# Kernel tuning notes

Hardware: AMD Instinct MI355X
Metric: run time of the kernel (lower is better)

## Reference

```python
import jax, jax.numpy as jnp
import numpy as np

NUM_CLS = 80
SR = 0.2
STRIDES = (8, 16, 32, 64, 128)
IMG = 1280
FMAPS = [(IMG // s, IMG // s) for s in STRIDES]
MAX_BOXES = 128
BIG_AREA = 1e7  # padding value for box-area argmin (matches tf.pad constant)


def _shrink_boxes(boxes, fw, fh, stride, sr):
    # shrink gt boxes by `sr` around their center and snap to feature-grid ints
    b = boxes / stride
    cx = (b[:, 0] + b[:, 2]) * 0.5
    cy = (b[:, 1] + b[:, 3]) * 0.5
    hw = (b[:, 2] - b[:, 0]) * sr * 0.5
    hh = (b[:, 3] - b[:, 1]) * sr * 0.5
    px1 = jnp.clip(jnp.floor(cx - hw), 0, fw - 1).astype(jnp.int32)
    py1 = jnp.clip(jnp.floor(cy - hh), 0, fh - 1).astype(jnp.int32)
    px2 = jnp.clip(jnp.ceil(cx + hw).astype(jnp.int32), px1 + 1, fw)
    py2 = jnp.clip(jnp.ceil(cy + hh).astype(jnp.int32), py1 + 1, fh)
    return px1, py1, px2, py2


def _level_targets(boxes, labels, valid, sel_w, fh, fw, stride):
    # Vectorized replacement of the per-box tf.map_fn + tf.pad + argmin + gather_nd.
    # The original builds a padded dense map per box; padding values are:
    #   cls one-hot -> 0, soft weight -> 1, regr mask -> 0, regr target -> 0, area -> 1e7.
    # We instead compute dense [K,fh,fw] maps and mask, which is the same math.
    px1, py1, px2, py2 = _shrink_boxes(boxes, fw, fh, stride, SR)  # [K]
    sx = (jnp.arange(fw, dtype=jnp.float32) + 0.5) * stride  # pixel-center x
    sy = (jnp.arange(fh, dtype=jnp.float32) + 0.5) * stride  # pixel-center y
    dl = jnp.maximum(sx[None, None, :] - boxes[:, 0, None, None], 0.0)  # [K,fh,fw]
    dt = jnp.maximum(sy[None, :, None] - boxes[:, 1, None, None], 0.0)
    dr = jnp.maximum(boxes[:, 2, None, None] - sx[None, None, :], 0.0)
    db = jnp.maximum(boxes[:, 3, None, None] - sy[None, :, None], 0.0)
    gx = jnp.arange(fw)[None, None, :]
    gy = jnp.arange(fh)[None, :, None]
    in_box = ((gx >= px1[:, None, None]) & (gx < px2[:, None, None])
              & (gy >= py1[:, None, None]) & (gy < py2[:, None, None])
              & valid[:, None, None])  # [K,fh,fw] positive region per box
    area = jnp.where(in_box, (dl + dr) * (dt + db), BIG_AREA)
    win = jnp.argmin(area, axis=0)  # [fh,fw] smallest-area box per pixel

    take = lambda a: jnp.take_along_axis(a, win[None], axis=0)[0]
    is_pos = take(in_box).astype(jnp.float32)
    dl_w, dt_w, dr_w, db_w = take(dl), take(dt), take(dr), take(db)

    # anchor-point weight min/max ratio (guard 0/0 which is only hit off-target)
    num = jnp.minimum(dl_w, dr_w) * jnp.minimum(dt_w, db_w)
    den = jnp.maximum(dl_w, dr_w) * jnp.maximum(dt_w, db_w)
    ap = jnp.where(den > 0, num / jnp.maximum(den, 1e-12), 0.0)
    soft = jnp.where(is_pos > 0, ap * sel_w[win], 1.0)

    onehot = jax.nn.one_hot(labels[win], NUM_CLS, dtype=jnp.float32) * is_pos[..., None]
    regr = (jnp.stack([dl_w, dt_w, dr_w, db_w], axis=-1) / (4.0 * stride)) * is_pos[..., None]
    extra = jnp.stack([soft, is_pos], axis=-1)  # [fh,fw,2] soft weight + pos mask
    cls_t = jnp.concatenate([onehot, extra], axis=-1).reshape(fh * fw, NUM_CLS + 2)
    regr_t = jnp.concatenate([regr, extra], axis=-1).reshape(fh * fw, 4 + 2)
    return cls_t, regr_t


def reference(gt_boxes, feature_select_weight, feature_maps_shape):
    # feature_maps_shape is accepted for signature fidelity; shapes must be
    # static under jit so we use the FMAPS constant (same values).
    labels = gt_boxes[:, 4].astype(jnp.int32)
    boxes = gt_boxes[:, :4]
    valid = jnp.any(jnp.abs(boxes) > 0, axis=1)  # trim_zero_padding_boxes as mask
    cls_list, regr_list = [], []
    for lvl, stride in enumerate(STRIDES):
        fh, fw = FMAPS[lvl]
        c, r = _level_targets(boxes, labels, valid,
                              feature_select_weight[:, lvl], fh, fw, stride)
        cls_list.append(c)
        regr_list.append(r)
    return jnp.concatenate(cls_list, axis=0), jnp.concatenate(regr_list, axis=0)


def setup_inputs():
    key = jax.random.key(0)
    k1, k2, k3, k4 = jax.random.split(key, 4)
    xy = jax.random.uniform(k1, (MAX_BOXES, 2), minval=0.0, maxval=IMG - 64.0)
    wh = jax.random.uniform(k2, (MAX_BOXES, 2), minval=32.0, maxval=420.0)
    x2y2 = jnp.minimum(xy + wh, IMG - 1.0)
    labels = jax.random.randint(k3, (MAX_BOXES, 1), 0, NUM_CLS).astype(jnp.float32)
    gt = jnp.concatenate([xy, x2y2, labels], axis=-1)
    # zero out last quarter to exercise the zero-padding trim path
    pad_mask = (jnp.arange(MAX_BOXES) < MAX_BOXES * 3 // 4).astype(jnp.float32)
    gt = gt * pad_mask[:, None]
    fsw = jax.random.uniform(k4, (MAX_BOXES, len(STRIDES)))
    fshape = jnp.array(FMAPS, dtype=jnp.int32)
    return {"gt_boxes": gt, "feature_select_weight": fsw,
            "feature_maps_shape": fshape}
```

## Files before the change

kernel.cpp:

```cpp
#include <hip/hip_runtime.h>
#include <math.h>
#include <limits.h>

#define NUM_CLS   80
#define MAX_BOXES 128
#define NLVL      5
#define BIG_AREA  1.0e7f
#define TOTAL_PIX 34100
#define PPB       128

__global__ __launch_bounds__(256) void fcos_targets_kernel(
    const float* __restrict__ gt,
    const float* __restrict__ fsw,
    float* __restrict__ out_cls,
    float* __restrict__ out_reg)
{
    __shared__ float4 sbx[MAX_BOXES];
    __shared__ int4   sshr[MAX_BOXES][NLVL];
    __shared__ float  ssw[MAX_BOXES][NLVL];
    __shared__ int    slab[MAX_BOXES];
    __shared__ float  pbest[PPB];
    __shared__ int    pwin[PPB];
    __shared__ float  st_soft[PPB];
    __shared__ float  st_ispos[PPB];
    __shared__ int    st_lab[PPB];
    __shared__ float  st_reg[PPB][4];

    const int t = threadIdx.x;
    const int block_base = blockIdx.x * PPB;
    const int block_last = min(block_base + PPB, TOTAL_PIX) - 1;

    const int lvl_lo = (block_base < 25600) ? 0 : (block_base < 32000) ? 1 :
                       (block_base < 33600) ? 2 : (block_base < 34000) ? 3 : 4;
    const int lvl_hi = (block_last < 25600) ? 0 : (block_last < 32000) ? 1 :
                       (block_last < 33600) ? 2 : (block_last < 34000) ? 3 : 4;

    if (t < MAX_BOXES) {
        const float x1 = gt[t * 5 + 0];
        const float y1 = gt[t * 5 + 1];
        const float x2 = gt[t * 5 + 2];
        const float y2 = gt[t * 5 + 3];
        sbx[t]  = make_float4(x1, y1, x2, y2);
        slab[t] = (int)gt[t * 5 + 4];
        const bool valid = (fabsf(x1) > 0.f) || (fabsf(y1) > 0.f) ||
                           (fabsf(x2) > 0.f) || (fabsf(y2) > 0.f);
        for (int l = lvl_lo; l <= lvl_hi; ++l) {
            const float inv_s = 1.0f / (float)(8 << l);
            const int   fw    = 160 >> l;
            const float fwm1  = (float)(fw - 1);
            const float bx1 = x1 * inv_s, by1 = y1 * inv_s;
            const float bx2 = x2 * inv_s, by2 = y2 * inv_s;
            const float cx = (bx1 + bx2) * 0.5f;
            const float cy = (by1 + by2) * 0.5f;
            const float hw = ((bx2 - bx1) * 0.2f) * 0.5f;
            const float hh = ((by2 - by1) * 0.2f) * 0.5f;
            int px1 = (int)fminf(fmaxf(floorf(cx - hw), 0.f), fwm1);
            int py1 = (int)fminf(fmaxf(floorf(cy - hh), 0.f), fwm1);
            int px2 = min(max((int)ceilf(cx + hw), px1 + 1), fw);
            int py2 = min(max((int)ceilf(cy + hh), py1 + 1), fw);
            if (!valid) { px1 = INT_MAX; py1 = INT_MAX; px2 = 0; py2 = 0; }
            sshr[t][l] = make_int4(px1, py1, px2, py2);
        }
    } else {
        const int b = t - MAX_BOXES;
        #pragma unroll
        for (int l = 0; l < NLVL; ++l) ssw[b][l] = fsw[b * NLVL + l];
    }
    __syncthreads();

    const int count = min(PPB, TOTAL_PIX - block_base);
    const int p   = t & (PPB - 1);
    const int pid = block_base + p;
    const bool active = (p < count);

    float best = BIG_AREA;
    int   win  = (t < PPB) ? 0 : 64;
    int   lvl = 0, gx = 0, gy = 0;
    float sx = 0.f, sy = 0.f;

    if (active) {
        int fw, lp; float stride;
        if      (pid < 25600) { lvl = 0; fw = 160; lp = pid;         stride = 8.f;   }
        else if (pid < 32000) { lvl = 1; fw = 80;  lp = pid - 25600; stride = 16.f;  }
        else if (pid < 33600) { lvl = 2; fw = 40;  lp = pid - 32000; stride = 32.f;  }
        else if (pid < 34000) { lvl = 3; fw = 20;  lp = pid - 33600; stride = 64.f;  }
        else                  { lvl = 4; fw = 10;  lp = pid - 34000; stride = 128.f; }
        gy = lp / fw;
        gx = lp - gy * fw;
        sx = ((float)gx + 0.5f) * stride;
        sy = ((float)gy + 0.5f) * stride;

        const int i0 = (t < PPB) ? 0 : 64;
        for (int j = 0; j < 64; ++j) {
            const int i = i0 + j;
            const int4  s = sshr[i][lvl];
            const float4 b = sbx[i];
            const bool inb = (gx >= s.x) & (gx < s.z) & (gy >= s.y) & (gy < s.w);
            const float dl = fmaxf(sx - b.x, 0.f);
            const float dt = fmaxf(sy - b.y, 0.f);
            const float dr = fmaxf(b.z - sx, 0.f);
            const float db = fmaxf(b.w - sy, 0.f);
            const float area = inb ? (dl + dr) * (dt + db) : BIG_AREA;
            if (area < best) { best = area; win = i; }
        }
    }
    if (t >= PPB) { pbest[p] = best; pwin[p] = win; }
    __syncthreads();

    if (t < PPB && active) {
        const float b2 = pbest[p];
        if (b2 < best) { best = b2; win = pwin[p]; }

        const int4   s = sshr[win][lvl];
        const float4 b = sbx[win];
        const bool inb = (gx >= s.x) & (gx < s.z) & (gy >= s.y) & (gy < s.w);
        const float dl = fmaxf(sx - b.x, 0.f);
        const float dt = fmaxf(sy - b.y, 0.f);
        const float dr = fmaxf(b.z - sx, 0.f);
        const float db = fmaxf(b.w - sy, 0.f);

        const float is_pos = inb ? 1.0f : 0.0f;
        const float num = fminf(dl, dr) * fminf(dt, db);
        const float den = fmaxf(dl, dr) * fmaxf(dt, db);
        const float ap  = (den > 0.f) ? num / fmaxf(den, 1e-12f) : 0.0f;
        const float soft = inb ? ap * ssw[win][lvl] : 1.0f;

        const float rs = 0.25f / (float)(8 << lvl);
        st_soft[p]  = soft;
        st_ispos[p] = is_pos;
        st_lab[p]   = slab[win];
        st_reg[p][0] = dl * rs * is_pos;
        st_reg[p][1] = dt * rs * is_pos;
        st_reg[p][2] = dr * rs * is_pos;
        st_reg[p][3] = db * rs * is_pos;
    }
    __syncthreads();

    if (count == PPB) {
        float4* cp = (float4*)(out_cls + (size_t)block_base * (NUM_CLS + 2));
        for (int q = t; q < PPB * (NUM_CLS + 2) / 4; q += 256) {
            const int flat = q * 4;
            const int row0 = (int)((unsigned)flat / 82u);
            const int col0 = flat - row0 * 82;
            float v[4];
            #pragma unroll
            for (int k = 0; k < 4; ++k) {
                int r = row0, c = col0 + k;
                if (c >= 82) { c -= 82; ++r; }
                const float ip = st_ispos[r];
                float val;
                if (c < NUM_CLS)       val = (c == st_lab[r] && ip != 0.f) ? 1.0f : 0.0f;
                else if (c == NUM_CLS) val = st_soft[r];
                else                   val = ip;
                v[k] = val;
            }
            cp[q] = make_float4(v[0], v[1], v[2], v[3]);
        }
        float4* rp = (float4*)(out_reg + (size_t)block_base * 6);
        for (int q = t; q < PPB * 6 / 4; q += 256) {
            const int flat = q * 4;
            const int row0 = (int)((unsigned)flat / 6u);
            const int col0 = flat - row0 * 6;
            float v[4];
            #pragma unroll
            for (int k = 0; k < 4; ++k) {
                int r = row0, c = col0 + k;
                if (c >= 6) { c -= 6; ++r; }
                v[k] = (c < 4) ? st_reg[r][c] : ((c == 4) ? st_soft[r] : st_ispos[r]);
            }
            rp[q] = make_float4(v[0], v[1], v[2], v[3]);
        }
    } else {
        float* cbase = out_cls + (size_t)block_base * (NUM_CLS + 2);
        for (int q = t; q < count * (NUM_CLS + 2); q += 256) {
            const int r = (int)((unsigned)q / 82u);
            const int c = q - r * 82;
            const float ip = st_ispos[r];
            float val;
            if (c < NUM_CLS)       val = (c == st_lab[r] && ip != 0.f) ? 1.0f : 0.0f;
            else if (c == NUM_CLS) val = st_soft[r];
            else                   val = ip;
            cbase[q] = val;
        }
        float* rbase = out_reg + (size_t)block_base * 6;
        for (int q = t; q < count * 6; q += 256) {
            const int r = (int)((unsigned)q / 6u);
            const int c = q - r * 6;
            rbase[q] = (c < 4) ? st_reg[r][c] : ((c == 4) ? st_soft[r] : st_ispos[r]);
        }
    }
}

extern "C" void kernel_launch(void* const* d_in, const int* in_sizes, int n_in,
                              void* d_out, int out_size, void* d_ws, size_t ws_size,
                              hipStream_t stream) {
    (void)in_sizes; (void)n_in; (void)out_size; (void)d_ws; (void)ws_size;
    const float* gt  = (const float*)d_in[0];
    const float* fsw = (const float*)d_in[1];
    float* out_cls = (float*)d_out;
    float* out_reg = out_cls + (size_t)TOTAL_PIX * (NUM_CLS + 2);

    const int blocks = (TOTAL_PIX + PPB - 1) / PPB;
    fcos_targets_kernel<<<blocks, 256, 0, stream>>>(gt, fsw, out_cls, out_reg);
}
```

Before: 70.83 us.

## Replace per-pixel box scan with box-to-pixel atomicMin scatter

Instead of each pixel testing all 128 boxes, each (box, level) pair scatters its shrunk region's areas into a workspace via 64-bit atomicMin on a packed (area, box index) key. A gather kernel then reads the winning box per pixel and writes outputs. This removes the dense K×pixels scan, since shrunk regions are small, but adds two extra kernel launches, a workspace init pass and atomic traffic. Ties resolve to the lowest box index, which matches argmin.

```diff
diff --git a/kernel.cpp b/kernel.cpp
--- a/kernel.cpp
+++ b/kernel.cpp
@@ -9,18 +9,90 @@
 #define TOTAL_PIX 34100
 #define PPB       128
 
-__global__ __launch_bounds__(256) void fcos_targets_kernel(
+#define INIT_KEY  0x4B18968000000000ULL
+
+__device__ __forceinline__ int level_base(int lvl) {
+    switch (lvl) {
+        case 0:  return 0;
+        case 1:  return 25600;
+        case 2:  return 32000;
+        case 3:  return 33600;
+        default: return 34000;
+    }
+}
+
+__global__ __launch_bounds__(256) void init_winner(unsigned long long* __restrict__ w) {
+    const int i = blockIdx.x * 256 + threadIdx.x;
+    if (i < TOTAL_PIX) w[i] = INIT_KEY;
+}
+
+__global__ __launch_bounds__(256) void scatter_kernel(
+    const float* __restrict__ gt,
+    unsigned long long* __restrict__ w)
+{
+    const int gtid = blockIdx.x * 256 + threadIdx.x;
+    const int pair = gtid >> 6;
+    const int lane = threadIdx.x & 63;
+    if (pair >= MAX_BOXES * NLVL) return;
+    const int box = pair & (MAX_BOXES - 1);
+    const int lvl = pair >> 7;
+
+    const float x1 = gt[box * 5 + 0];
+    const float y1 = gt[box * 5 + 1];
+    const float x2 = gt[box * 5 + 2];
+    const float y2 = gt[box * 5 + 3];
+    const bool valid = (fabsf(x1) > 0.f) || (fabsf(y1) > 0.f) ||
+                       (fabsf(x2) > 0.f) || (fabsf(y2) > 0.f);
+    if (!valid) return;
+
+    const float stride = (float)(8 << lvl);
+    const float inv_s  = 1.0f / stride;
+    const int   fw     = 160 >> lvl;
+    const float fwm1   = (float)(fw - 1);
+
+    const float bx1 = x1 * inv_s, by1 = y1 * inv_s;
+    const float bx2 = x2 * inv_s, by2 = y2 * inv_s;
+    const float cx = (bx1 + bx2) * 0.5f;
+    const float cy = (by1 + by2) * 0.5f;
+    const float hw = ((bx2 - bx1) * 0.2f) * 0.5f;
+    const float hh = ((by2 - by1) * 0.2f) * 0.5f;
+    const int px1 = (int)fminf(fmaxf(floorf(cx - hw), 0.f), fwm1);
+    const int py1 = (int)fminf(fmaxf(floorf(cy - hh), 0.f), fwm1);
+    const int px2 = min(max((int)ceilf(cx + hw), px1 + 1), fw);
+    const int py2 = min(max((int)ceilf(cy + hh), py1 + 1), fw);
+
+    const int rw = px2 - px1;
+    const int n  = rw * (py2 - py1);
+    const int base = level_base(lvl);
+
+    for (int i = lane; i < n; i += 64) {
+        const int ry = i / rw;
+        const int rx = i - ry * rw;
+        const int gx = px1 + rx;
+        const int gy = py1 + ry;
+        const float sx = ((float)gx + 0.5f) * stride;
+        const float sy = ((float)gy + 0.5f) * stride;
+        const float dl = fmaxf(sx - x1, 0.f);
+        const float dt = fmaxf(sy - y1, 0.f);
+        const float dr = fmaxf(x2 - sx, 0.f);
+        const float db = fmaxf(y2 - sy, 0.f);
+        const float area = (dl + dr) * (dt + db);
+        const unsigned long long key =
+            ((unsigned long long)__float_as_uint(area) << 32) | (unsigned)box;
+        atomicMin(&w[base + gy * fw + gx], key);
+    }
+}
+
+__global__ __launch_bounds__(256) void gather_kernel(
     const float* __restrict__ gt,
     const float* __restrict__ fsw,
+    const unsigned long long* __restrict__ w,
     float* __restrict__ out_cls,
     float* __restrict__ out_reg)
 {
     __shared__ float4 sbx[MAX_BOXES];
-    __shared__ int4   sshr[MAX_BOXES][NLVL];
     __shared__ float  ssw[MAX_BOXES][NLVL];
     __shared__ int    slab[MAX_BOXES];
-    __shared__ float  pbest[PPB];
-    __shared__ int    pwin[PPB];
     __shared__ float  st_soft[PPB];
     __shared__ float  st_ispos[PPB];
     __shared__ int    st_lab[PPB];
@@ -28,12 +100,6 @@
 
     const int t = threadIdx.x;
     const int block_base = blockIdx.x * PPB;
-    const int block_last = min(block_base + PPB, TOTAL_PIX) - 1;
-
-    const int lvl_lo = (block_base < 25600) ? 0 : (block_base < 32000) ? 1 :
-                       (block_base < 33600) ? 2 : (block_base < 34000) ? 3 : 4;
-    const int lvl_hi = (block_last < 25600) ? 0 : (block_last < 32000) ? 1 :
-                       (block_last < 33600) ? 2 : (block_last < 34000) ? 3 : 4;
 
     if (t < MAX_BOXES) {
         const float x1 = gt[t * 5 + 0];
@@ -42,25 +108,6 @@
         const float y2 = gt[t * 5 + 3];
         sbx[t]  = make_float4(x1, y1, x2, y2);
         slab[t] = (int)gt[t * 5 + 4];
-        const bool valid = (fabsf(x1) > 0.f) || (fabsf(y1) > 0.f) ||
-                           (fabsf(x2) > 0.f) || (fabsf(y2) > 0.f);
-        for (int l = lvl_lo; l <= lvl_hi; ++l) {
-            const float inv_s = 1.0f / (float)(8 << l);
-            const int   fw    = 160 >> l;
-            const float fwm1  = (float)(fw - 1);
-            const float bx1 = x1 * inv_s, by1 = y1 * inv_s;
-            const float bx2 = x2 * inv_s, by2 = y2 * inv_s;
-            const float cx = (bx1 + bx2) * 0.5f;
-            const float cy = (by1 + by2) * 0.5f;
-            const float hw = ((bx2 - bx1) * 0.2f) * 0.5f;
-            const float hh = ((by2 - by1) * 0.2f) * 0.5f;
-            int px1 = (int)fminf(fmaxf(floorf(cx - hw), 0.f), fwm1);
-            int py1 = (int)fminf(fmaxf(floorf(cy - hh), 0.f), fwm1);
-            int px2 = min(max((int)ceilf(cx + hw), px1 + 1), fw);
-            int py2 = min(max((int)ceilf(cy + hh), py1 + 1), fw);
-            if (!valid) { px1 = INT_MAX; py1 = INT_MAX; px2 = 0; py2 = 0; }
-            sshr[t][l] = make_int4(px1, py1, px2, py2);
-        }
     } else {
         const int b = t - MAX_BOXES;
         #pragma unroll
@@ -69,70 +116,44 @@
     __syncthreads();
 
     const int count = min(PPB, TOTAL_PIX - block_base);
-    const int p   = t & (PPB - 1);
-    const int pid = block_base + p;
-    const bool active = (p < count);
-
-    float best = BIG_AREA;
-    int   win  = (t < PPB) ? 0 : 64;
-    int   lvl = 0, gx = 0, gy = 0;
-    float sx = 0.f, sy = 0.f;
-
-    if (active) {
-        int fw, lp; float stride;
+
+    if (t < PPB && t < count) {
+        const int pid = block_base + t;
+        int lvl, fw, lp; float stride;
         if      (pid < 25600) { lvl = 0; fw = 160; lp = pid;         stride = 8.f;   }
         else if (pid < 32000) { lvl = 1; fw = 80;  lp = pid - 25600; stride = 16.f;  }
         else if (pid < 33600) { lvl = 2; fw = 40;  lp = pid - 32000; stride = 32.f;  }
         else if (pid < 34000) { lvl = 3; fw = 20;  lp = pid - 33600; stride = 64.f;  }
         else                  { lvl = 4; fw = 10;  lp = pid - 34000; stride = 128.f; }
-        gy = lp / fw;
-        gx = lp - gy * fw;
-        sx = ((float)gx + 0.5f) * stride;
-        sy = ((float)gy + 0.5f) * stride;
-
-        const int i0 = (t < PPB) ? 0 : 64;
-        for (int j = 0; j < 64; ++j) {
-            const int i = i0 + j;
-            const int4  s = sshr[i][lvl];
-            const float4 b = sbx[i];
-            const bool inb = (gx >= s.x) & (gx < s.z) & (gy >= s.y) & (gy < s.w);
-            const float dl = fmaxf(sx - b.x, 0.f);
-            const float dt = fmaxf(sy - b.y, 0.f);
-            const float dr = fmaxf(b.z - sx, 0.f);
-            const float db = fmaxf(b.w - sy, 0.f);
-            const float area = inb ? (dl + dr) * (dt + db) : BIG_AREA;
-            if (area < best) { best = area; win = i; }
-        }
-    }
-    if (t >= PPB) { pbest[p] = best; pwin[p] = win; }
-    __syncthreads();
-
-    if (t < PPB && active) {
-        const float b2 = pbest[p];
-        if (b2 < best) { best = b2; win = pwin[p]; }
-
-        const int4   s = sshr[win][lvl];
+        const int gy = lp / fw;
+        const int gx = lp - gy * fw;
+        const float sx = ((float)gx + 0.5f) * stride;
+        const float sy = ((float)gy + 0.5f) * stride;
+
+        const unsigned long long key = w[pid];
+        const bool pos = key < INIT_KEY;
+        const int  win = (int)(unsigned)key;
+
         const float4 b = sbx[win];
-        const bool inb = (gx >= s.x) & (gx < s.z) & (gy >= s.y) & (gy < s.w);
         const float dl = fmaxf(sx - b.x, 0.f);
         const float dt = fmaxf(sy - b.y, 0.f);
         const float dr = fmaxf(b.z - sx, 0.f);
         const float db = fmaxf(b.w - sy, 0.f);
 
-        const float is_pos = inb ? 1.0f : 0.0f;
+        const float is_pos = pos ? 1.0f : 0.0f;
         const float num = fminf(dl, dr) * fminf(dt, db);
         const float den = fmaxf(dl, dr) * fmaxf(dt, db);
         const float ap  = (den > 0.f) ? num / fmaxf(den, 1e-12f) : 0.0f;
-        const float soft = inb ? ap * ssw[win][lvl] : 1.0f;
-
-        const float rs = 0.25f / (float)(8 << lvl);
-        st_soft[p]  = soft;
-        st_ispos[p] = is_pos;
-        st_lab[p]   = slab[win];
-        st_reg[p][0] = dl * rs * is_pos;
-        st_reg[p][1] = dt * rs * is_pos;
-        st_reg[p][2] = dr * rs * is_pos;
-        st_reg[p][3] = db * rs * is_pos;
+        const float soft = pos ? ap * ssw[win][lvl] : 1.0f;
+
+        const float rs = 0.25f / stride;
+        st_soft[t]  = soft;
+        st_ispos[t] = is_pos;
+        st_lab[t]   = slab[win];
+        st_reg[t][0] = dl * rs * is_pos;
+        st_reg[t][1] = dt * rs * is_pos;
+        st_reg[t][2] = dr * rs * is_pos;
+        st_reg[t][3] = db * rs * is_pos;
     }
     __syncthreads();
 
@@ -194,12 +215,14 @@
 extern "C" void kernel_launch(void* const* d_in, const int* in_sizes, int n_in,
                               void* d_out, int out_size, void* d_ws, size_t ws_size,
                               hipStream_t stream) {
-    (void)in_sizes; (void)n_in; (void)out_size; (void)d_ws; (void)ws_size;
+    (void)in_sizes; (void)n_in; (void)out_size; (void)ws_size;
     const float* gt  = (const float*)d_in[0];
     const float* fsw = (const float*)d_in[1];
     float* out_cls = (float*)d_out;
     float* out_reg = out_cls + (size_t)TOTAL_PIX * (NUM_CLS + 2);
-
-    const int blocks = (TOTAL_PIX + PPB - 1) / PPB;
-    fcos_targets_kernel<<<blocks, 256, 0, stream>>>(gt, fsw, out_cls, out_reg);
-}
+    unsigned long long* w = (unsigned long long*)d_ws;
+
+    init_winner  <<<(TOTAL_PIX + 255) / 256, 256, 0, stream>>>(w);
+    scatter_kernel<<<(MAX_BOXES * NLVL * 64 + 255) / 256, 256, 0, stream>>>(gt, w);
+    gather_kernel<<<(TOTAL_PIX + PPB - 1) / PPB, 256, 0, stream>>>(gt, fsw, w, out_cls, out_reg);
+}
```

Result: no change. 69.44 us, median of 2 (-2.0%).
